# Optimization experiments

Measured on AMD Instinct MI355X. Metric: run time of the kernel, lower is better.

## Reference

```python
import jax, jax.numpy as jnp
import numpy as np


def setup_inputs() -> dict:
    key = jax.random.key(0)
    B, S, I, H, O = 32, 2048, 128, 512, 128
    ks = jax.random.split(key, 24)
    sc = 0.05
    d = {
        "x": jax.random.normal(ks[0], (B, S, I), jnp.float32),
        "h0": jnp.zeros((B, 2, H), jnp.float32),
        "l0_wxz": jax.random.normal(ks[1], (H, I)) * sc,
        "l0_bxz": jax.random.normal(ks[2], (H,)) * sc,
        "l0_whz": jax.random.normal(ks[3], (H, H)) * sc,
        "l0_wxr": jax.random.normal(ks[4], (H, I)) * sc,
        "l0_bxr": jax.random.normal(ks[5], (H,)) * sc,
        "l0_whr": jax.random.normal(ks[6], (H, H)) * sc,
        "l0_wxg": jax.random.normal(ks[7], (H, I)) * sc,
        "l0_bxg": jax.random.normal(ks[8], (H,)) * sc,
        "l0_whg": jax.random.normal(ks[9], (H, H)) * sc,
        "l1_wxz": jax.random.normal(ks[10], (H, H)) * sc,
        "l1_bxz": jax.random.normal(ks[11], (H,)) * sc,
        "l1_whz": jax.random.normal(ks[12], (H, H)) * sc,
        "l1_wxr": jax.random.normal(ks[13], (H, H)) * sc,
        "l1_bxr": jax.random.normal(ks[14], (H,)) * sc,
        "l1_whr": jax.random.normal(ks[15], (H, H)) * sc,
        "l1_wxg": jax.random.normal(ks[16], (H, H)) * sc,
        "l1_bxg": jax.random.normal(ks[17], (H,)) * sc,
        "l1_whg": jax.random.normal(ks[18], (H, H)) * sc,
        "wy": jax.random.normal(ks[19], (O, H)) * sc,
        "by": jax.random.normal(ks[20], (O,)) * sc,
    }
    return d


def _gru_cell(xt, h, wxz, bxz, whz, wxr, bxr, whr, wxg, bxg, whg):
    # z = sigmoid(Wxz x + bxz + Whz h); r = sigmoid(...); g = tanh(Wxg x + bxg + Whg (r*h))
    z = jax.nn.sigmoid(xt @ wxz.T + bxz + h @ whz.T)
    r = jax.nn.sigmoid(xt @ wxr.T + bxr + h @ whr.T)
    g = jnp.tanh(xt @ wxg.T + bxg + (r * h) @ whg.T)
    return z * h + (1.0 - z) * g


def reference(x, h0,
              l0_wxz, l0_bxz, l0_whz, l0_wxr, l0_bxr, l0_whr, l0_wxg, l0_bxg, l0_whg,
              l1_wxz, l1_bxz, l1_whz, l1_wxr, l1_bxr, l1_whr, l1_wxg, l1_bxg, l1_whg,
              wy, by):
    p0 = (l0_wxz, l0_bxz, l0_whz, l0_wxr, l0_bxr, l0_whr, l0_wxg, l0_bxg, l0_whg)
    p1 = (l1_wxz, l1_bxz, l1_whz, l1_wxr, l1_bxr, l1_whr, l1_wxg, l1_bxg, l1_whg)

    def step(carry, xt):  # xt: (B, I)
        h0_, h1_ = carry
        h0n = _gru_cell(xt, h0_, *p0)
        h1n = _gru_cell(h0n, h1_, *p1)
        y = h1n @ wy.T + by
        return (h0n, h1n), y

    xs = jnp.swapaxes(x, 0, 1)  # (S, B, I)
    init = (h0[:, 0, :], h0[:, 1, :])
    (hf0, hf1), ys = jax.lax.scan(step, init, xs)
    layer_output = jnp.swapaxes(ys, 0, 1)  # (B, S, O)
    hidden_state = jnp.stack([hf0, hf1], axis=1)  # (B, L, H)
    return layer_output, hidden_state
```

## Files before the change

### kernel.cpp

```cpp
#include <hip/hip_runtime.h>
#include <math.h>

typedef __bf16 bf16x8 __attribute__((ext_vector_type(8)));
typedef float f32x4 __attribute__((ext_vector_type(4)));
typedef unsigned short u16;
typedef unsigned int u32;
typedef unsigned long long u64;

#define MFMA16(a, b, c) __builtin_amdgcn_mfma_f32_16x16x32_bf16((a), (b), (c), 0, 0, 0)

namespace {
constexpr int kB = 32, kS = 2048, kI = 128, kH = 512, kO = 128;
constexpr int NC = 2;
constexpr int BPC = 16;
constexpr int L0WG = 16;
constexpr int WGC = 48;
constexpr int NT = 2 * kS + 3;
constexpr long LOUT = (long)kB * kS * kO;

constexpr size_t WS_FLG  = 0;
constexpr size_t WS_PUB0 = 8192;
constexpr size_t WS_PUB1 = WS_PUB0 + (size_t)NC * 2 * BPC * kH * 2;
constexpr size_t WS_PR0  = WS_PUB1 + (size_t)NC * 2 * BPC * kH * 2;
constexpr size_t WS_PR1  = WS_PR0  + (size_t)NC * 2 * BPC * kH * 2;
constexpr size_t WS_WTS  = WS_PR1  + (size_t)NC * 2 * BPC * kH * 2;

constexpr int W0H = 0;
constexpr int W0X = 786432;
constexpr int W1X = 983040;
constexpr int W1H = 1769472;
constexpr int WYO = 2555904;

constexpr int HP = 520;
constexpr int IP = 136;
}

__device__ __forceinline__ u16 f2bf(float f) {
  u32 x = __float_as_uint(f);
  return (u16)((x + 0x7fffu + ((x >> 16) & 1u)) >> 16);
}

__global__ void prep_kernel(const float* whz0, const float* whr0, const float* whg0,
                            const float* wxz0, const float* wxr0, const float* wxg0,
                            const float* wxz1, const float* wxr1, const float* wxg1,
                            const float* whz1, const float* whr1, const float* whg1,
                            const float* wy, const float* h0in, char* ws) {
  u16* wts = (u16*)(ws + WS_WTS);
  int gid = blockIdx.x * blockDim.x + threadIdx.x;
  int stride = gridDim.x * blockDim.x;
  for (int i = gid; i < 786432; i += stride) {
    int g = i >> 18, r = i & 262143;
    wts[W0H + i] = f2bf((g == 0 ? whz0 : g == 1 ? whr0 : whg0)[r]);
  }
  for (int i = gid; i < 196608; i += stride) {
    int g = i >> 16, r = i & 65535;
    wts[W0X + i] = f2bf((g == 0 ? wxz0 : g == 1 ? wxr0 : wxg0)[r]);
  }
  for (int i = gid; i < 786432; i += stride) {
    int g = i >> 18, r = i & 262143;
    wts[W1X + i] = f2bf((g == 0 ? wxz1 : g == 1 ? wxr1 : wxg1)[r]);
  }
  for (int i = gid; i < 786432; i += stride) {
    int g = i >> 18, r = i & 262143;
    wts[W1H + i] = f2bf((g == 0 ? whz1 : g == 1 ? whr1 : whg1)[r]);
  }
  for (int i = gid; i < 65536; i += stride) wts[WYO + i] = f2bf(wy[i]);

  u16* p0 = (u16*)(ws + WS_PUB0);
  u16* p1 = (u16*)(ws + WS_PUB1);
  for (int i = gid; i < NC * BPC * kH; i += stride) {
    int c = i / (BPC * kH), rem = i - c * (BPC * kH);
    int b = rem / kH, k = rem - b * kH;
    int bg = c * BPC + b;
    p0[(c * 2 + 1) * BPC * kH + rem] = f2bf(h0in[(size_t)bg * 2 * kH + k]);
    p1[(c * 2 + 1) * BPC * kH + rem] = f2bf(h0in[(size_t)bg * 2 * kH + kH + k]);
  }
  if (gid < 2048) ((u32*)(ws + WS_FLG))[gid] = 0u;
}

__device__ __forceinline__ void stage_c(u16* dst, const u16* src) {
  u64* s = (u64*)src;
  int t = threadIdx.x;
#pragma unroll
  for (int j = 0; j < 8; ++j) {
    int idx = j * 256 + t;
    u64 v = __hip_atomic_load(s + idx, __ATOMIC_RELAXED, __HIP_MEMORY_SCOPE_AGENT);
    int b = idx >> 7, i = idx & 127;
    *(u64*)(dst + b * HP + i * 4) = v;
  }
}
__device__ __forceinline__ void stage_c_half(u16* dst, const u16* src, int lt) {
  u64* s = (u64*)src;
#pragma unroll
  for (int j = 0; j < 16; ++j) {
    int idx = j * 128 + lt;
    u64 v = __hip_atomic_load(s + idx, __ATOMIC_RELAXED, __HIP_MEMORY_SCOPE_AGENT);
    int b = idx >> 7, i = idx & 127;
    *(u64*)(dst + b * HP + i * 4) = v;
  }
}

__device__ __forceinline__ void st_tile(float* base, f32x4 c, int q, int li) {
#pragma unroll
  for (int r = 0; r < 4; ++r) base[(q * 4 + r) * 17 + li] = c[r];
}

__device__ __forceinline__ void pub2(u16* base, int off, float v0, float v1) {
  u32 pk = (u32)f2bf(v0) | ((u32)f2bf(v1) << 16);
  __hip_atomic_store((u32*)(base + off), pk, __ATOMIC_RELAXED, __HIP_MEMORY_SCOPE_AGENT);
}

__device__ __forceinline__ float sigm(float x) { return 1.f / (1.f + __expf(-x)); }
__device__ __forceinline__ float tanh_f(float x) {
  float te = __expf(-2.f * fabsf(x));
  return __builtin_copysignf((1.f - te) / (1.f + te), x);
}

__device__ __forceinline__ void cbar(u32* flags, int wid, u32 target) {
  __syncthreads();
  if (threadIdx.x == 0)
    __hip_atomic_store(&flags[wid * 16], target, __ATOMIC_RELAXED, __HIP_MEMORY_SCOPE_AGENT);
  if (threadIdx.x < WGC) {
    while (__hip_atomic_load(&flags[threadIdx.x * 16], __ATOMIC_RELAXED,
                             __HIP_MEMORY_SCOPE_AGENT) < target)
      __builtin_amdgcn_s_sleep(1);
  }
  __syncthreads();
}

__global__ __launch_bounds__(256, 1)
void gru_kernel(const float* __restrict__ xg, const float* __restrict__ h0in,
                const float* __restrict__ bxz0, const float* __restrict__ bxr0,
                const float* __restrict__ bxg0, const float* __restrict__ bxz1,
                const float* __restrict__ bxr1, const float* __restrict__ bxg1,
                const float* __restrict__ byv, float* __restrict__ out, char* ws) {
  const int cl = blockIdx.x / WGC;
  const int wid = blockIdx.x - cl * WGC;
  const bool isL0 = wid < L0WG;
  const int w0 = wid, w1 = wid - L0WG;
  const int tid = threadIdx.x;
  const int lane = tid & 63, wv = tid >> 6;
  const int q = lane >> 4, li = lane & 15;
  const int kh = wv & 1;
  const int nt = wv >> 1;
  const bool xside = wv < 2;

  u16* pub0 = (u16*)(ws + WS_PUB0) + (size_t)cl * 2 * BPC * kH;
  u16* pub1 = (u16*)(ws + WS_PUB1) + (size_t)cl * 2 * BPC * kH;
  u16* pr0  = (u16*)(ws + WS_PR0)  + (size_t)cl * 2 * BPC * kH;
  u16* pr1  = (u16*)(ws + WS_PR1)  + (size_t)cl * 2 * BPC * kH;
  const u16* wts = (const u16*)(ws + WS_WTS);
  u32* flags = (u32*)(ws + WS_FLG) + (size_t)cl * 1024;

  __shared__ __align__(16) char smem[57216];
  u16* h0buf = (u16*)smem;
  u16* h1buf = (u16*)(smem + 16640);
  u16* xbuf  = (u16*)(smem + 16640);
  u16* rhbuf = (u16*)smem;
  float* spA = (float*)(smem + 33280);
  float* spB = (float*)(smem + 33280);
  float* ypA = (float*)(smem + 55040);

  bf16x8 wA[3][8];
  bf16x8 wE[8];
  if (isL0) {
    const int ci = w0 * 32 + nt * 16 + li;
#pragma unroll
    for (int g = 0; g < 3; ++g)
#pragma unroll
      for (int s = 0; s < 8; ++s)
        wA[g][s] = *(const bf16x8*)(wts + W0H + ((size_t)(g * kH + ci) * kH + kh * 256 + q * 8 + s * 32));
#pragma unroll
    for (int g = 0; g < 3; ++g)
#pragma unroll
      for (int s = 0; s < 2; ++s)
        wE[g * 2 + s] = *(const bf16x8*)(wts + W0X + ((size_t)(g * kH + ci) * kI + kh * 64 + q * 8 + s * 32));
  } else {
    const int ci = w1 * 16 + li;
    const int base = xside ? W1X : W1H;
#pragma unroll
    for (int g = 0; g < 3; ++g)
#pragma unroll
      for (int s = 0; s < 8; ++s)
        wA[g][s] = *(const bf16x8*)(wts + base + ((size_t)(g * kH + ci) * kH + kh * 256 + q * 8 + s * 32));
    if (!xside && w1 < 8) {
#pragma unroll
      for (int s = 0; s < 8; ++s)
        wE[s] = *(const bf16x8*)(wts + WYO + ((size_t)ci * kH + kh * 256 + q * 8 + s * 32));
    }
  }

  float2 bz2 = {0.f, 0.f}, br2 = {0.f, 0.f}, bg2 = {0.f, 0.f};
  float by_r = 0.f;
  float hm0r = 0.f, hm1r = 0.f;
  float zA0 = 0.f, zA1 = 0.f, gA0 = 0.f, gA1 = 0.f;
  if (isL0) {
    const int c0i = (tid & 15) * 2, bq = tid >> 4;
    bz2 = *(const float2*)(bxz0 + w0 * 32 + c0i);
    br2 = *(const float2*)(bxr0 + w0 * 32 + c0i);
    bg2 = *(const float2*)(bxg0 + w0 * 32 + c0i);
    const float* hp = h0in + (size_t)(cl * 16 + bq) * 2 * kH + w0 * 32 + c0i;
    hm0r = hp[0]; hm1r = hp[1];
  } else {
    const int c0i = (tid & 7) * 2, bq = tid >> 3;
    bz2 = *(const float2*)(bxz1 + w1 * 16 + c0i);
    br2 = *(const float2*)(bxr1 + w1 * 16 + c0i);
    bg2 = *(const float2*)(bxg1 + w1 * 16 + c0i);
    if (bq < 16) {
      const float* hp = h0in + (size_t)(cl * 16 + bq) * 2 * kH + kH + w1 * 16 + c0i;
      hm0r = hp[0]; hm1r = hp[1];
    }
    if (w1 < 8) by_r = byv[w1 * 16 + (tid & 15)];
  }

  for (int tk = 0; tk < NT; ++tk) {
    const bool ev = (tk & 1) == 0;
    const int t = tk >> 1;
    const int u = t - 1;
    const bool l0A = isL0 && ev && t < kS;
    const bool l0B = isL0 && !ev && t < kS;
    const bool l1A = !isL0 && ev && t >= 1 && t <= kS;
    const bool l1B = !isL0 && !ev && t >= 1 && t <= kS;
    const bool stH1 = !isL0 && ev && t >= 1 && t <= kS + 1;
    const bool yAct = !isL0 && ev && w1 < 8 && t >= 2 && t <= kS + 1;

    if (l0A) {
      stage_c(h0buf, pub0 + ((t - 1) & 1) * BPC * kH);
      int b = tid >> 4, i0 = (tid & 15) * 8;
      const float* xr = xg + ((size_t)(cl * 16 + b) * kS + t) * kI + i0;
      float4 v0 = *(const float4*)xr;
      float4 v1 = *(const float4*)(xr + 4);
      int4 pk;
      pk.x = (int)((u32)f2bf(v0.x) | ((u32)f2bf(v0.y) << 16));
      pk.y = (int)((u32)f2bf(v0.z) | ((u32)f2bf(v0.w) << 16));
      pk.z = (int)((u32)f2bf(v1.x) | ((u32)f2bf(v1.y) << 16));
      pk.w = (int)((u32)f2bf(v1.z) | ((u32)f2bf(v1.w) << 16));
      *(int4*)(xbuf + b * IP + i0) = pk;
    }
    if (!isL0 && ev) {
      if (tid < 128) {
        if (l1A) stage_c_half(h0buf, pub0 + (u & 1) * BPC * kH, tid);
      } else {
        if (stH1) stage_c_half(h1buf, pub1 + ((u - 1) & 1) * BPC * kH, tid - 128);
      }
    }
    if (l0B) stage_c(rhbuf, pr0 + (t & 1) * BPC * kH);
    if (l1B) stage_c(rhbuf, pr1 + (u & 1) * BPC * kH);
    __syncthreads();

    if (l0A) {
      f32x4 hz = {0.f, 0.f, 0.f, 0.f}, hr = hz, xz = hz, xr2 = hz, xg2 = hz;
      const u16* ap = h0buf + li * HP + kh * 256 + q * 8;
#pragma unroll
      for (int s = 0; s < 8; ++s) {
        bf16x8 a = *(const bf16x8*)(ap + s * 32);
        hz = MFMA16(a, wA[0][s], hz);
        hr = MFMA16(a, wA[1][s], hr);
      }
      const u16* xp = xbuf + li * IP + kh * 64 + q * 8;
#pragma unroll
      for (int s = 0; s < 2; ++s) {
        bf16x8 a = *(const bf16x8*)(xp + s * 32);
        xz  = MFMA16(a, wE[0 + s], xz);
        xr2 = MFMA16(a, wE[2 + s], xr2);
        xg2 = MFMA16(a, wE[4 + s], xg2);
      }
      st_tile(spA + ((0 * 2 + nt) * 2 + kh) * 272, hz, q, li);
      st_tile(spA + ((1 * 2 + nt) * 2 + kh) * 272, hr, q, li);
      st_tile(spA + ((2 * 2 + nt) * 2 + kh) * 272, xz, q, li);
      st_tile(spA + ((3 * 2 + nt) * 2 + kh) * 272, xr2, q, li);
      st_tile(spA + ((4 * 2 + nt) * 2 + kh) * 272, xg2, q, li);
    } else if (!isL0 && ev) {
      if (xside) {
        if (l1A) {
          f32x4 cz = {0.f, 0.f, 0.f, 0.f}, cr = cz, cg = cz;
          const u16* ap = h0buf + li * HP + kh * 256 + q * 8;
#pragma unroll
          for (int s = 0; s < 8; ++s) {
            bf16x8 a = *(const bf16x8*)(ap + s * 32);
            cz = MFMA16(a, wA[0][s], cz);
            cr = MFMA16(a, wA[1][s], cr);
            cg = MFMA16(a, wA[2][s], cg);
          }
          st_tile(spA + (2 * 2 + kh) * 272, cz, q, li);
          st_tile(spA + (3 * 2 + kh) * 272, cr, q, li);
          st_tile(spA + (4 * 2 + kh) * 272, cg, q, li);
        }
      } else {
        const bool rec = t >= 1 && t <= kS;
        const bool ym = (w1 < 8) && t >= 2 && t <= kS + 1;
        if (rec || ym) {
          f32x4 cz = {0.f, 0.f, 0.f, 0.f}, cr = cz, cy = cz;
          const u16* ap = h1buf + li * HP + kh * 256 + q * 8;
#pragma unroll
          for (int s = 0; s < 8; ++s) {
            bf16x8 a = *(const bf16x8*)(ap + s * 32);
            if (rec) {
              cz = MFMA16(a, wA[0][s], cz);
              cr = MFMA16(a, wA[1][s], cr);
            }
            if (ym) cy = MFMA16(a, wE[s], cy);
          }
          if (rec) {
            st_tile(spA + (0 * 2 + kh) * 272, cz, q, li);
            st_tile(spA + (1 * 2 + kh) * 272, cr, q, li);
          }
          if (ym) st_tile(ypA + kh * 272, cy, q, li);
        }
      }
    } else if (l0B) {
      f32x4 cg = {0.f, 0.f, 0.f, 0.f};
      const u16* ap = rhbuf + li * HP + kh * 256 + q * 8;
#pragma unroll
      for (int s = 0; s < 8; ++s)
        cg = MFMA16(*(const bf16x8*)(ap + s * 32), wA[2][s], cg);
      st_tile(spB + (nt * 2 + kh) * 272, cg, q, li);
    } else if (l1B && !xside) {
      f32x4 cg = {0.f, 0.f, 0.f, 0.f};
      const u16* ap = rhbuf + li * HP + kh * 256 + q * 8;
#pragma unroll
      for (int s = 0; s < 8; ++s)
        cg = MFMA16(*(const bf16x8*)(ap + s * 32), wA[2][s], cg);
      st_tile(spB + kh * 272, cg, q, li);
    }
    __syncthreads();

    if (l0A) {
      const int cp = tid & 15, b = tid >> 4;
      const int c0 = cp * 2, n2 = c0 >> 4, cc = c0 & 15, o = b * 17 + cc;
      float hz0 = spA[((0*2+n2)*2+0)*272 + o] + spA[((0*2+n2)*2+1)*272 + o];
      float hz1 = spA[((0*2+n2)*2+0)*272 + o+1] + spA[((0*2+n2)*2+1)*272 + o+1];
      float hr0 = spA[((1*2+n2)*2+0)*272 + o] + spA[((1*2+n2)*2+1)*272 + o];
      float hr1 = spA[((1*2+n2)*2+0)*272 + o+1] + spA[((1*2+n2)*2+1)*272 + o+1];
      float xz0 = spA[((2*2+n2)*2+0)*272 + o] + spA[((2*2+n2)*2+1)*272 + o];
      float xz1 = spA[((2*2+n2)*2+0)*272 + o+1] + spA[((2*2+n2)*2+1)*272 + o+1];
      float xr0 = spA[((3*2+n2)*2+0)*272 + o] + spA[((3*2+n2)*2+1)*272 + o];
      float xr1 = spA[((3*2+n2)*2+0)*272 + o+1] + spA[((3*2+n2)*2+1)*272 + o+1];
      float xg0 = spA[((4*2+n2)*2+0)*272 + o] + spA[((4*2+n2)*2+1)*272 + o];
      float xg1 = spA[((4*2+n2)*2+0)*272 + o+1] + spA[((4*2+n2)*2+1)*272 + o+1];
      zA0 = sigm(hz0 + xz0 + bz2.x);
      zA1 = sigm(hz1 + xz1 + bz2.y);
      float r0 = sigm(hr0 + xr0 + br2.x);
      float r1 = sigm(hr1 + xr1 + br2.y);
      gA0 = xg0 + bg2.x;
      gA1 = xg1 + bg2.y;
      pub2(pr0 + (t & 1) * BPC * kH, b * kH + w0 * 32 + c0, r0 * hm0r, r1 * hm1r);
    }
    if (l1A && tid < 128) {
      const int cp = tid & 7, b = tid >> 3;
      const int c0 = cp * 2, o = b * 17 + c0;
      float hz0 = spA[(0*2+0)*272 + o] + spA[(0*2+1)*272 + o];
      float hz1 = spA[(0*2+0)*272 + o+1] + spA[(0*2+1)*272 + o+1];
      float hr0 = spA[(1*2+0)*272 + o] + spA[(1*2+1)*272 + o];
      float hr1 = spA[(1*2+0)*272 + o+1] + spA[(1*2+1)*272 + o+1];
      float xz0 = spA[(2*2+0)*272 + o] + spA[(2*2+1)*272 + o];
      float xz1 = spA[(2*2+0)*272 + o+1] + spA[(2*2+1)*272 + o+1];
      float xr0 = spA[(3*2+0)*272 + o] + spA[(3*2+1)*272 + o];
      float xr1 = spA[(3*2+0)*272 + o+1] + spA[(3*2+1)*272 + o+1];
      float xg0 = spA[(4*2+0)*272 + o] + spA[(4*2+1)*272 + o];
      float xg1 = spA[(4*2+0)*272 + o+1] + spA[(4*2+1)*272 + o+1];
      zA0 = sigm(hz0 + xz0 + bz2.x);
      zA1 = sigm(hz1 + xz1 + bz2.y);
      float r0 = sigm(hr0 + xr0 + br2.x);
      float r1 = sigm(hr1 + xr1 + br2.y);
      gA0 = xg0 + bg2.x;
      gA1 = xg1 + bg2.y;
      pub2(pr1 + (u & 1) * BPC * kH, b * kH + w1 * 16 + c0, r0 * hm0r, r1 * hm1r);
    }
    if (yAct) {
      const int c = tid & 15, b = tid >> 4;
      float y = ypA[b * 17 + c] + ypA[272 + b * 17 + c] + by_r;
      out[((size_t)(cl * 16 + b) * kS + (t - 2)) * kO + w1 * 16 + c] = y;
    }
    if (l0B) {
      const int cp = tid & 15, b = tid >> 4;
      const int c0 = cp * 2, n2 = c0 >> 4, cc = c0 & 15, o = b * 17 + cc;
      float gh0 = spB[(n2*2+0)*272 + o] + spB[(n2*2+1)*272 + o];
      float gh1 = spB[(n2*2+0)*272 + o+1] + spB[(n2*2+1)*272 + o+1];
      float g0 = tanh_f(gA0 + gh0), g1 = tanh_f(gA1 + gh1);
      float hn0 = zA0 * hm0r + (1.f - zA0) * g0;
      float hn1 = zA1 * hm1r + (1.f - zA1) * g1;
      hm0r = hn0; hm1r = hn1;
      pub2(pub0 + (t & 1) * BPC * kH, b * kH + w0 * 32 + c0, hn0, hn1);
      if (t == kS - 1) {
        float* op = out + LOUT + (size_t)(cl * 16 + b) * 2 * kH + w0 * 32 + c0;
        op[0] = hn0; op[1] = hn1;
      }
    }
    if (l1B && tid < 128) {
      const int cp = tid & 7, b = tid >> 3;
      const int c0 = cp * 2, o = b * 17 + c0;
      float gh0 = spB[0 * 272 + o] + spB[1 * 272 + o];
      float gh1 = spB[0 * 272 + o+1] + spB[1 * 272 + o+1];
      float g0 = tanh_f(gA0 + gh0), g1 = tanh_f(gA1 + gh1);
      float hn0 = zA0 * hm0r + (1.f - zA0) * g0;
      float hn1 = zA1 * hm1r + (1.f - zA1) * g1;
      hm0r = hn0; hm1r = hn1;
      pub2(pub1 + (u & 1) * BPC * kH, b * kH + w1 * 16 + c0, hn0, hn1);
      if (u == kS - 1) {
        float* op = out + LOUT + (size_t)(cl * 16 + b) * 2 * kH + kH + w1 * 16 + c0;
        op[0] = hn0; op[1] = hn1;
      }
    }

    if (tk != NT - 1) cbar(flags, wid, (u32)(tk + 1));
  }
}

extern "C" void kernel_launch(void* const* d_in, const int* in_sizes, int n_in,
                              void* d_out, int out_size, void* d_ws, size_t ws_size,
                              hipStream_t stream) {
  (void)in_sizes; (void)n_in; (void)out_size; (void)ws_size;
  const float* x      = (const float*)d_in[0];
  const float* h0     = (const float*)d_in[1];
  const float* l0_wxz = (const float*)d_in[2];
  const float* l0_bxz = (const float*)d_in[3];
  const float* l0_whz = (const float*)d_in[4];
  const float* l0_wxr = (const float*)d_in[5];
  const float* l0_bxr = (const float*)d_in[6];
  const float* l0_whr = (const float*)d_in[7];
  const float* l0_wxg = (const float*)d_in[8];
  const float* l0_bxg = (const float*)d_in[9];
  const float* l0_whg = (const float*)d_in[10];
  const float* l1_wxz = (const float*)d_in[11];
  const float* l1_bxz = (const float*)d_in[12];
  const float* l1_whz = (const float*)d_in[13];
  const float* l1_wxr = (const float*)d_in[14];
  const float* l1_bxr = (const float*)d_in[15];
  const float* l1_whr = (const float*)d_in[16];
  const float* l1_wxg = (const float*)d_in[17];
  const float* l1_bxg = (const float*)d_in[18];
  const float* l1_whg = (const float*)d_in[19];
  const float* wy     = (const float*)d_in[20];
  const float* by     = (const float*)d_in[21];
  float* out = (float*)d_out;
  char* ws = (char*)d_ws;

  prep_kernel<<<512, 256, 0, stream>>>(l0_whz, l0_whr, l0_whg, l0_wxz, l0_wxr, l0_wxg,
                                       l1_wxz, l1_wxr, l1_wxg, l1_whz, l1_whr, l1_whg,
                                       wy, h0, ws);
  gru_kernel<<<NC * WGC, 256, 0, stream>>>(x, h0, l0_bxz, l0_bxr, l0_bxg,
                                           l1_bxz, l1_bxr, l1_bxg, by, out, ws);
}
```

Baseline: 19.62 ms.

## Replace global cluster barrier with layer-specific flag waits and deeper h0 buffering

Replaces the all-to-all barrier across the 48 workgroups of a cluster with targeted waits. Layer-0 workgroups now wait only on other layer-0 workgroups, plus a lagged check on layer-1. Layer-1 workgroups wait on layer-1 and, on odd phases, on layer-0. The layer-0 hidden-state publish buffer grows from double to quadruple buffering so layer 0 can run a few steps ahead of layer 1 without overwriting data still being read. This cuts barrier latency and decouples the two layers, at the cost of subtle ordering correctness that relies on the lag bound.

Measured after the change: 24.79 ms. 26.3% more time.

```diff
diff --git a/kernel.cpp b/kernel.cpp
--- a/kernel.cpp
+++ b/kernel.cpp
@@ -20,7 +20,7 @@
 
 constexpr size_t WS_FLG  = 0;
 constexpr size_t WS_PUB0 = 8192;
-constexpr size_t WS_PUB1 = WS_PUB0 + (size_t)NC * 2 * BPC * kH * 2;
+constexpr size_t WS_PUB1 = WS_PUB0 + (size_t)NC * 4 * BPC * kH * 2;
 constexpr size_t WS_PR0  = WS_PUB1 + (size_t)NC * 2 * BPC * kH * 2;
 constexpr size_t WS_PR1  = WS_PR0  + (size_t)NC * 2 * BPC * kH * 2;
 constexpr size_t WS_WTS  = WS_PR1  + (size_t)NC * 2 * BPC * kH * 2;
@@ -72,7 +72,7 @@
     int c = i / (BPC * kH), rem = i - c * (BPC * kH);
     int b = rem / kH, k = rem - b * kH;
     int bg = c * BPC + b;
-    p0[(c * 2 + 1) * BPC * kH + rem] = f2bf(h0in[(size_t)bg * 2 * kH + k]);
+    p0[(c * 4 + 3) * BPC * kH + rem] = f2bf(h0in[(size_t)bg * 2 * kH + k]);
     p1[(c * 2 + 1) * BPC * kH + rem] = f2bf(h0in[(size_t)bg * 2 * kH + kH + k]);
   }
   if (gid < 2048) ((u32*)(ws + WS_FLG))[gid] = 0u;
@@ -114,18 +114,6 @@
 __device__ __forceinline__ float tanh_f(float x) {
   float te = __expf(-2.f * fabsf(x));
   return __builtin_copysignf((1.f - te) / (1.f + te), x);
-}
-
-__device__ __forceinline__ void cbar(u32* flags, int wid, u32 target) {
-  __syncthreads();
-  if (threadIdx.x == 0)
-    __hip_atomic_store(&flags[wid * 16], target, __ATOMIC_RELAXED, __HIP_MEMORY_SCOPE_AGENT);
-  if (threadIdx.x < WGC) {
-    while (__hip_atomic_load(&flags[threadIdx.x * 16], __ATOMIC_RELAXED,
-                             __HIP_MEMORY_SCOPE_AGENT) < target)
-      __builtin_amdgcn_s_sleep(1);
-  }
-  __syncthreads();
 }
 
 __global__ __launch_bounds__(256, 1)
@@ -145,12 +133,13 @@
   const int nt = wv >> 1;
   const bool xside = wv < 2;
 
-  u16* pub0 = (u16*)(ws + WS_PUB0) + (size_t)cl * 2 * BPC * kH;
+  u16* pub0 = (u16*)(ws + WS_PUB0) + (size_t)cl * 4 * BPC * kH;
   u16* pub1 = (u16*)(ws + WS_PUB1) + (size_t)cl * 2 * BPC * kH;
   u16* pr0  = (u16*)(ws + WS_PR0)  + (size_t)cl * 2 * BPC * kH;
   u16* pr1  = (u16*)(ws + WS_PR1)  + (size_t)cl * 2 * BPC * kH;
   const u16* wts = (const u16*)(ws + WS_WTS);
-  u32* flags = (u32*)(ws + WS_FLG) + (size_t)cl * 1024;
+  u32* flags0 = (u32*)(ws + WS_FLG) + (size_t)cl * 1024;
+  u32* flags1 = flags0 + 16;
 
   __shared__ __align__(16) char smem[57216];
   u16* h0buf = (u16*)smem;
@@ -225,7 +214,7 @@
     const bool yAct = !isL0 && ev && w1 < 8 && t >= 2 && t <= kS + 1;
 
     if (l0A) {
-      stage_c(h0buf, pub0 + ((t - 1) & 1) * BPC * kH);
+      stage_c(h0buf, pub0 + ((t - 1) & 3) * BPC * kH);
       int b = tid >> 4, i0 = (tid & 15) * 8;
       const float* xr = xg + ((size_t)(cl * 16 + b) * kS + t) * kI + i0;
       float4 v0 = *(const float4*)xr;
@@ -239,7 +228,7 @@
     }
     if (!isL0 && ev) {
       if (tid < 128) {
-        if (l1A) stage_c_half(h0buf, pub0 + (u & 1) * BPC * kH, tid);
+        if (l1A) stage_c_half(h0buf, pub0 + (u & 3) * BPC * kH, tid);
       } else {
         if (stH1) stage_c_half(h1buf, pub1 + ((u - 1) & 1) * BPC * kH, tid - 128);
       }
@@ -381,7 +370,7 @@
       float hn0 = zA0 * hm0r + (1.f - zA0) * g0;
       float hn1 = zA1 * hm1r + (1.f - zA1) * g1;
       hm0r = hn0; hm1r = hn1;
-      pub2(pub0 + (t & 1) * BPC * kH, b * kH + w0 * 32 + c0, hn0, hn1);
+      pub2(pub0 + (t & 3) * BPC * kH, b * kH + w0 * 32 + c0, hn0, hn1);
       if (t == kS - 1) {
         float* op = out + LOUT + (size_t)(cl * 16 + b) * 2 * kH + w0 * 32 + c0;
         op[0] = hn0; op[1] = hn1;
@@ -403,7 +392,33 @@
       }
     }
 
-    if (tk != NT - 1) cbar(flags, wid, (u32)(tk + 1));
+    if (tk != NT - 1) {
+      __syncthreads();
+      if (tid == 0) {
+        u32* myf = isL0 ? &flags0[w0] : &flags1[w1];
+        __hip_atomic_store(myf, (u32)(tk + 1), __ATOMIC_RELAXED, __HIP_MEMORY_SCOPE_AGENT);
+      }
+      u32 t0 = 0, t1 = 0;
+      if (isL0) {
+        t0 = (u32)(tk + 1);
+        if (ev && tk >= 6) t1 = (u32)(tk - 5);
+      } else {
+        t1 = (u32)(tk + 1);
+        if (!ev) t0 = (u32)(tk + 1);
+      }
+      if (tid < 16) {
+        if (t0)
+          while (__hip_atomic_load(&flags0[tid], __ATOMIC_RELAXED,
+                                   __HIP_MEMORY_SCOPE_AGENT) < t0)
+            __builtin_amdgcn_s_sleep(1);
+      } else if (tid < 48) {
+        if (t1)
+          while (__hip_atomic_load(&flags1[tid - 16], __ATOMIC_RELAXED,
+                                   __HIP_MEMORY_SCOPE_AGENT) < t1)
+            __builtin_amdgcn_s_sleep(1);
+      }
+      __syncthreads();
+    }
   }
 }
 
```
